# Performance work log

Measured on AMD Instinct MI355X. Metric: run time of the kernel, lower is better.

Reference implementation:

```python
import jax, jax.numpy as jnp
import numpy as np

N = 1_000_000   # total points across all frames in batch
B = 8           # frames (segments) per batch
C = 256         # bottleneck / backbone_out_channels
H = 512         # lstm_hidden_channels
NUM_CLASSES = 20


def setup_inputs() -> dict:
    key = jax.random.key(0)
    ks = jax.random.split(key, 10)
    s = lambda k, shape, scale=0.02: jax.random.normal(k, shape, dtype=jnp.float32) * scale
    feat = jax.random.normal(ks[0], (N, C), dtype=jnp.float32)
    # cumulative offsets: equal-size segments ending at N (torch offset convention)
    offset = (jnp.arange(1, B + 1, dtype=jnp.int32) * (N // B)).astype(jnp.int32)
    return {
        "feat": feat,
        "offset": offset,
        "W_ih": s(ks[1], (4 * H, C)),
        "b_ih": s(ks[2], (4 * H,)),
        "W_hh": s(ks[3], (4 * H, H)),
        "b_hh": s(ks[4], (4 * H,)),
        "W_proj": s(ks[5], (C, H)),
        "b_proj": s(ks[6], (C,)),
        "W_head": s(ks[7], (NUM_CLASSES, C)),
        "b_head": s(ks[8], (NUM_CLASSES,)),
    }


def reference(feat, offset, W_ih, b_ih, W_hh, b_hh, W_proj, b_proj, W_head, b_head):
    n = feat.shape[0]
    # --- ragged per-segment mean pooling (replaces Python loop over offsets) ---
    seg_id = jnp.searchsorted(offset, jnp.arange(n, dtype=offset.dtype), side="right")
    counts = offset - jnp.concatenate([jnp.zeros((1,), offset.dtype), offset[:-1]])
    sums = jax.ops.segment_sum(feat, seg_id, num_segments=offset.shape[0])  # [B, C]
    pooled = sums / counts[:, None].astype(feat.dtype)                      # [B, C]
    # --- LSTMCell with zero initial (h, c): torch gate order i, f, g, o ---
    gates = pooled @ W_ih.T + b_ih + b_hh                                   # h0 = 0 -> W_hh term drops
    i, f, g, o = jnp.split(gates, 4, axis=-1)
    c = jax.nn.sigmoid(i) * jnp.tanh(g)                                     # f * c0 = 0
    h = jax.nn.sigmoid(o) * jnp.tanh(c)                                     # [B, H]
    _ = jax.nn.sigmoid(f)  # f gate unused with zero cell state (kept implicit)
    # --- temporal projection + broadcast fuse (dropout p=0 in eval) ---
    ctx = h @ W_proj.T + b_proj                                             # [B, C]
    fused = feat + ctx[seg_id]                                              # [N, C]
    # --- segmentation head ---
    seg_logits = fused @ W_head.T + b_head                                  # [N, num_classes]
    return seg_logits
```

## Files before the change

### kernel.cpp

```cpp
#include <hip/hip_runtime.h>
#include <math.h>

#define CDIM 256
#define HDIM 512
#define KCLS 20
#define MAXSEG 8
#define TILE_R 64
#define NTHR 512
#define F4_TILE (TILE_R * CDIM / 4)
#define F4_THR (F4_TILE / NTHR)
#define GRIDA 512

__global__ __launch_bounds__(NTHR, 4) void fused_pool_head_kernel(
    const float* __restrict__ feat, const int* __restrict__ offset,
    const float* __restrict__ W_head, const float* __restrict__ b_head,
    float* __restrict__ sums, float* __restrict__ out, int n, int nseg) {
  __shared__ float tile[TILE_R * CDIM];
  float4* tile4 = (float4*)tile;
  int t = threadIdx.x;
  int lane = t & 63;
  int wv = t >> 6;

  int kb_ = (wv < 4) ? wv * 3 : 12 + (wv - 4) * 2;
  int kb = __builtin_amdgcn_readfirstlane(kb_);
  float bh0 = b_head[kb], bh1 = b_head[kb + 1];
  float bh2 = (wv < 4) ? b_head[kb + 2] : 0.f;

  int ntiles = (n + TILE_R - 1) / TILE_R;
  int nb = (int)gridDim.x;
  int t0 = (int)blockIdx.x;

  int off[MAXSEG];
#pragma unroll
  for (int q = 0; q < MAXSEG; ++q) off[q] = (q < nseg) ? offset[q] : 0x7fffffff;

  int col = t & 255;
  int rhalf = (t >> 8) * 32;
  int c4s = col >> 2, js = col & 3;
  float colacc = 0.f;
  int cur_seg = -1;

  const float4* src = (const float4*)feat;
  long lim = (long)n * (CDIM / 4);
  float4 stgA[F4_THR], stgB[F4_THR];

  auto issue = [&](float4* stg, int tl) {
    long base = (long)tl * F4_TILE;
    if (base + F4_TILE <= lim) {
#pragma unroll
      for (int i = 0; i < F4_THR; ++i) stg[i] = src[base + i * NTHR + t];
    } else {
#pragma unroll
      for (int i = 0; i < F4_THR; ++i) {
        long idx = base + i * NTHR + t;
        stg[i] = (idx < lim) ? src[idx] : make_float4(0.f, 0.f, 0.f, 0.f);
      }
    }
  };
  auto dswrite = [&](const float4* stg) {
#pragma unroll
    for (int i = 0; i < F4_THR; ++i) {
      int idx = i * NTHR + t;
      int rr = idx >> 6, c4 = idx & 63;
      tile4[rr * 64 + (c4 ^ (rr & 7))] = stg[i];
    }
  };
  auto compute = [&](int tl) {
    long r0 = (long)tl * TILE_R;
    int rows = (int)(((long)n - r0) < TILE_R ? ((long)n - r0) : TILE_R);

    int rlo = rhalf, rhi = rhalf + 32;
    if (rhi > rows) rhi = rows;
    if (rlo < rhi) {
      long ra = r0 + rlo, rb = r0 + rhi - 1;
      int s0 = 0, s1 = 0;
#pragma unroll
      for (int q = 0; q < MAXSEG - 1; ++q) {
        s0 += (ra >= off[q]) ? 1 : 0;
        s1 += (rb >= off[q]) ? 1 : 0;
      }
      if (s0 == s1) {
        if (s0 != cur_seg) {
          if (cur_seg >= 0) atomicAdd(&sums[cur_seg * CDIM + col], colacc);
          colacc = 0.f;
          cur_seg = s0;
        }
        float a = 0.f;
#pragma unroll 8
        for (int rr = rlo; rr < rhi; ++rr)
          a += tile[(rr * 64 + (c4s ^ (rr & 7))) * 4 + js];
        colacc += a;
      } else {
        for (int rr = rlo; rr < rhi; ++rr) {
          long r = r0 + rr;
          int s = 0;
#pragma unroll
          for (int q = 0; q < MAXSEG - 1; ++q) s += (r >= off[q]) ? 1 : 0;
          if (s != cur_seg) {
            if (cur_seg >= 0) atomicAdd(&sums[cur_seg * CDIM + col], colacc);
            colacc = 0.f;
            cur_seg = s;
          }
          colacc += tile[(rr * 64 + (c4s ^ (rr & 7))) * 4 + js];
        }
      }
    }

    if (lane < rows) {
      const float4* trow = tile4 + lane * 64;
      int l7 = lane & 7;
      if (wv < 4) {
        float a0 = bh0, a1 = bh1, a2 = bh2;
        const float* w0 = W_head + (kb + 0) * CDIM;
        const float* w1 = W_head + (kb + 1) * CDIM;
        const float* w2 = W_head + (kb + 2) * CDIM;
#pragma unroll 4
        for (int c4 = 0; c4 < 64; ++c4) {
          float4 f = trow[c4 ^ l7];
          int cb = c4 * 4;
          a0 = fmaf(f.x, w0[cb], a0); a1 = fmaf(f.x, w1[cb], a1); a2 = fmaf(f.x, w2[cb], a2);
          a0 = fmaf(f.y, w0[cb+1], a0); a1 = fmaf(f.y, w1[cb+1], a1); a2 = fmaf(f.y, w2[cb+1], a2);
          a0 = fmaf(f.z, w0[cb+2], a0); a1 = fmaf(f.z, w1[cb+2], a1); a2 = fmaf(f.z, w2[cb+2], a2);
          a0 = fmaf(f.w, w0[cb+3], a0); a1 = fmaf(f.w, w1[cb+3], a1); a2 = fmaf(f.w, w2[cb+3], a2);
        }
        float* orow = out + (r0 + lane) * KCLS + kb;
        orow[0] = a0; orow[1] = a1; orow[2] = a2;
      } else {
        float a0 = bh0, a1 = bh1;
        const float* w0 = W_head + (kb + 0) * CDIM;
        const float* w1 = W_head + (kb + 1) * CDIM;
#pragma unroll 4
        for (int c4 = 0; c4 < 64; ++c4) {
          float4 f = trow[c4 ^ l7];
          int cb = c4 * 4;
          a0 = fmaf(f.x, w0[cb], a0);   a1 = fmaf(f.x, w1[cb], a1);
          a0 = fmaf(f.y, w0[cb+1], a0); a1 = fmaf(f.y, w1[cb+1], a1);
          a0 = fmaf(f.z, w0[cb+2], a0); a1 = fmaf(f.z, w1[cb+2], a1);
          a0 = fmaf(f.w, w0[cb+3], a0); a1 = fmaf(f.w, w1[cb+3], a1);
        }
        float* orow = out + (r0 + lane) * KCLS + kb;
        orow[0] = a0; orow[1] = a1;
      }
    }
  };

  if (t0 < ntiles) issue(stgA, t0);
  if (t0 + nb < ntiles) issue(stgB, t0 + nb);
  if (t0 < ntiles) dswrite(stgA);
  __syncthreads();

  for (int tl = t0; tl < ntiles; tl += 2 * nb) {
    int tA2 = tl + 2 * nb;
    if (tA2 < ntiles) issue(stgA, tA2);
    compute(tl);
    __syncthreads();
    int tB = tl + nb;
    if (tB < ntiles) dswrite(stgB);
    __syncthreads();
    if (tB < ntiles) {
      int tB2 = tl + 3 * nb;
      if (tB2 < ntiles) issue(stgB, tB2);
      compute(tB);
      __syncthreads();
      if (tA2 < ntiles) dswrite(stgA);
      __syncthreads();
    }
  }
  if (cur_seg >= 0) atomicAdd(&sums[cur_seg * CDIM + col], colacc);
}

__global__ __launch_bounds__(256) void lstm_h_kernel(
    const float* __restrict__ sums, const int* __restrict__ offset,
    const float* __restrict__ W_ih, const float* __restrict__ b_ih,
    const float* __restrict__ b_hh, float* __restrict__ h, int nseg) {
  __shared__ float pooled[MAXSEG * CDIM];
  int t = threadIdx.x;
  {
    int prev = 0;
    for (int s = 0; s < MAXSEG; ++s) {
      int cur = (s < nseg) ? offset[s] : prev;
      float cnt = (float)(cur - prev);
      float inv = (cnt > 0.f) ? 1.f / cnt : 0.f;
      pooled[s * CDIM + t] = sums[s * CDIM + t] * inv;
      prev = cur;
    }
  }
  __syncthreads();

  int wv = t >> 6, l = t & 63;
  int j = (int)blockIdx.x * 4 + wv;
  int s = l >> 3, ch = l & 7;

  const float4* Wi4 = (const float4*)(W_ih + (size_t)(0 * HDIM + j) * CDIM);
  const float4* Wg4 = (const float4*)(W_ih + (size_t)(2 * HDIM + j) * CDIM);
  const float4* Wo4 = (const float4*)(W_ih + (size_t)(3 * HDIM + j) * CDIM);
  const float4* p4 = (const float4*)(pooled + s * CDIM);

  float di = 0.f, dg = 0.f, dd = 0.f;
#pragma unroll
  for (int i = 0; i < 8; ++i) {
    int c4 = ch * 8 + i;
    float4 p = p4[c4];
    float4 wi = Wi4[c4], wg = Wg4[c4], wo = Wo4[c4];
    di = fmaf(p.x, wi.x, di); di = fmaf(p.y, wi.y, di);
    di = fmaf(p.z, wi.z, di); di = fmaf(p.w, wi.w, di);
    dg = fmaf(p.x, wg.x, dg); dg = fmaf(p.y, wg.y, dg);
    dg = fmaf(p.z, wg.z, dg); dg = fmaf(p.w, wg.w, dg);
    dd = fmaf(p.x, wo.x, dd); dd = fmaf(p.y, wo.y, dd);
    dd = fmaf(p.z, wo.z, dd); dd = fmaf(p.w, wo.w, dd);
  }
#pragma unroll
  for (int m = 1; m < 8; m <<= 1) {
    di += __shfl_xor(di, m);
    dg += __shfl_xor(dg, m);
    dd += __shfl_xor(dd, m);
  }
  if (ch == 0 && s < nseg) {
    di += b_ih[j] + b_hh[j];
    dg += b_ih[2 * HDIM + j] + b_hh[2 * HDIM + j];
    dd += b_ih[3 * HDIM + j] + b_hh[3 * HDIM + j];
    float ig = 1.f / (1.f + expf(-di));
    float gg = tanhf(dg);
    float og = 1.f / (1.f + expf(-dd));
    h[(size_t)s * HDIM + j] = og * tanhf(ig * gg);
  }
}

__global__ __launch_bounds__(256) void ctx_kernel(
    const float* __restrict__ h, const float* __restrict__ W_proj,
    const float* __restrict__ b_proj, float* __restrict__ ctx, int nseg) {
  __shared__ float hs[MAXSEG * HDIM];
  int t = threadIdx.x;
  {
    const float4* hsrc = (const float4*)h;
    float4* hdst = (float4*)hs;
#pragma unroll
    for (int i = 0; i < 4; ++i) hdst[i * 256 + t] = hsrc[i * 256 + t];
  }
  __syncthreads();

  int wv = t >> 6, l = t & 63;
  int col = (int)blockIdx.x * 4 + wv;
  int s = l >> 3, ch = l & 7;

  const float4* Wp4 = (const float4*)(W_proj + (size_t)col * HDIM);
  const float4* h4 = (const float4*)(hs + s * HDIM);
  float acc = 0.f;
#pragma unroll
  for (int i = 0; i < 16; ++i) {
    int j4 = ch * 16 + i;
    float4 hv = h4[j4];
    float4 w = Wp4[j4];
    acc = fmaf(hv.x, w.x, acc); acc = fmaf(hv.y, w.y, acc);
    acc = fmaf(hv.z, w.z, acc); acc = fmaf(hv.w, w.w, acc);
  }
#pragma unroll
  for (int m = 1; m < 8; m <<= 1) acc += __shfl_xor(acc, m);
  if (ch == 0 && s < nseg) ctx[s * CDIM + col] = acc + b_proj[col];
}

__global__ __launch_bounds__(256) void delta_kernel(
    const float* __restrict__ ctx, const float* __restrict__ W_head,
    float* __restrict__ delta, int nseg) {
  __shared__ float cs[MAXSEG * CDIM];
  int t = threadIdx.x;
  {
    const float4* csrc = (const float4*)ctx;
    float4* cdst = (float4*)cs;
#pragma unroll
    for (int i = 0; i < 2; ++i) cdst[i * 256 + t] = csrc[i * 256 + t];
  }
  __syncthreads();

  int wv = t >> 6, l = t & 63;
  int k = (int)blockIdx.x * 4 + wv;
  if (k >= KCLS) return;
  int s = l >> 3, ch = l & 7;

  const float4* Wh4 = (const float4*)(W_head + (size_t)k * CDIM);
  const float4* c4 = (const float4*)(cs + s * CDIM);
  float acc = 0.f;
#pragma unroll
  for (int i = 0; i < 8; ++i) {
    int idx = ch * 8 + i;
    float4 cv = c4[idx];
    float4 w = Wh4[idx];
    acc = fmaf(cv.x, w.x, acc); acc = fmaf(cv.y, w.y, acc);
    acc = fmaf(cv.z, w.z, acc); acc = fmaf(cv.w, w.w, acc);
  }
#pragma unroll
  for (int m = 1; m < 8; m <<= 1) acc += __shfl_xor(acc, m);
  if (ch == 0 && s < nseg) delta[s * KCLS + k] = acc;
}

__global__ __launch_bounds__(256) void add_delta_kernel(
    float* __restrict__ out, const int* __restrict__ offset,
    const float* __restrict__ delta, int n, int nseg) {
  __shared__ float dl[MAXSEG * KCLS];
  int t = threadIdx.x;
  if (t < MAXSEG * KCLS) dl[t] = (t < nseg * KCLS) ? delta[t] : 0.f;
  __syncthreads();

  int off[MAXSEG];
#pragma unroll
  for (int q = 0; q < MAXSEG; ++q) off[q] = (q < nseg) ? offset[q] : 0x7fffffff;

  long tot = (long)n * (KCLS / 4);
  long stride = (long)gridDim.x * 256;
  for (long e4 = (long)blockIdx.x * 256 + t; e4 < tot; e4 += stride) {
    long row = e4 / 5;
    int k0 = (int)(e4 - row * 5) * 4;
    int s = 0;
#pragma unroll
    for (int q = 0; q < MAXSEG - 1; ++q) s += (row >= off[q]) ? 1 : 0;
    float4 v = ((float4*)out)[e4];
    const float* d = &dl[s * KCLS + k0];
    v.x += d[0]; v.y += d[1]; v.z += d[2]; v.w += d[3];
    ((float4*)out)[e4] = v;
  }
}

extern "C" void kernel_launch(void* const* d_in, const int* in_sizes, int n_in,
                              void* d_out, int out_size, void* d_ws, size_t ws_size,
                              hipStream_t stream) {
  const float* feat   = (const float*)d_in[0];
  const int*   offset = (const int*)d_in[1];
  const float* W_ih   = (const float*)d_in[2];
  const float* b_ih   = (const float*)d_in[3];
  const float* b_hh   = (const float*)d_in[5];
  const float* W_proj = (const float*)d_in[6];
  const float* b_proj = (const float*)d_in[7];
  const float* W_head = (const float*)d_in[8];
  const float* b_head = (const float*)d_in[9];
  float* out = (float*)d_out;

  int n = in_sizes[0] / CDIM;
  int nseg = in_sizes[1];
  if (nseg > MAXSEG) nseg = MAXSEG;

  float* ws    = (float*)d_ws;
  float* sums  = ws;
  float* h     = ws + MAXSEG * CDIM;
  float* ctx   = ws + MAXSEG * CDIM + MAXSEG * HDIM;
  float* delta = ctx + MAXSEG * CDIM;

  hipMemsetAsync(sums, 0, MAXSEG * CDIM * sizeof(float), stream);
  fused_pool_head_kernel<<<GRIDA, NTHR, 0, stream>>>(feat, offset, W_head, b_head,
                                                     sums, out, n, nseg);
  lstm_h_kernel<<<128, 256, 0, stream>>>(sums, offset, W_ih, b_ih, b_hh, h, nseg);
  ctx_kernel<<<64, 256, 0, stream>>>(h, W_proj, b_proj, ctx, nseg);
  delta_kernel<<<5, 256, 0, stream>>>(ctx, W_head, delta, nseg);
  add_delta_kernel<<<2048, 256, 0, stream>>>(out, offset, delta, n, nseg);
}
```

Baseline: 367.5 us.

## Double-buffer LDS tiles with one barrier per tile and move pooling to four waves

Replaces the single LDS tile plus two register staging sets with two LDS buffers and one register stage. Each iteration now needs one barrier instead of two, and raw s_barrier/waitcnt calls are used. Column pooling moves off all eight waves onto waves 4-7 only, with float4 accumulation and a full-lane XOR swizzle. The fused kernel's grid drops to 256 blocks with the occupancy hint removed, and the add-delta grid grows to 2560 blocks. The doubled LDS footprint may limit how many blocks fit per CU, and the pooling work now sits unevenly across waves.

After: 681.1 us. 85.3% more time.

```diff
diff --git a/kernel.cpp b/kernel.cpp
--- a/kernel.cpp
+++ b/kernel.cpp
@@ -7,44 +7,54 @@
 #define MAXSEG 8
 #define TILE_R 64
 #define NTHR 512
+#define GRIDA 256
 #define F4_TILE (TILE_R * CDIM / 4)
 #define F4_THR (F4_TILE / NTHR)
-#define GRIDA 512
-
-__global__ __launch_bounds__(NTHR, 4) void fused_pool_head_kernel(
+
+__global__ __launch_bounds__(NTHR) void fused_pool_head_kernel(
     const float* __restrict__ feat, const int* __restrict__ offset,
     const float* __restrict__ W_head, const float* __restrict__ b_head,
     float* __restrict__ sums, float* __restrict__ out, int n, int nseg) {
-  __shared__ float tile[TILE_R * CDIM];
-  float4* tile4 = (float4*)tile;
+  __shared__ float4 tile4[2][F4_TILE];
   int t = threadIdx.x;
   int lane = t & 63;
   int wv = t >> 6;
+
+  int ntiles = (n + TILE_R - 1) / TILE_R;
+  int nb = (int)gridDim.x;
+  int t0 = (int)blockIdx.x;
+  if (t0 >= ntiles) return;
+
+  int off[MAXSEG];
+#pragma unroll
+  for (int q = 0; q < MAXSEG; ++q) off[q] = (q < nseg) ? offset[q] : 0x7fffffff;
 
   int kb_ = (wv < 4) ? wv * 3 : 12 + (wv - 4) * 2;
   int kb = __builtin_amdgcn_readfirstlane(kb_);
   float bh0 = b_head[kb], bh1 = b_head[kb + 1];
   float bh2 = (wv < 4) ? b_head[kb + 2] : 0.f;
 
-  int ntiles = (n + TILE_R - 1) / TILE_R;
-  int nb = (int)gridDim.x;
-  int t0 = (int)blockIdx.x;
-
-  int off[MAXSEG];
-#pragma unroll
-  for (int q = 0; q < MAXSEG; ++q) off[q] = (q < nseg) ? offset[q] : 0x7fffffff;
-
-  int col = t & 255;
-  int rhalf = (t >> 8) * 32;
-  int c4s = col >> 2, js = col & 3;
-  float colacc = 0.f;
+  int c4s = lane;
+  int rg = wv - 4;
+  float4 colacc = make_float4(0.f, 0.f, 0.f, 0.f);
   int cur_seg = -1;
 
   const float4* src = (const float4*)feat;
   long lim = (long)n * (CDIM / 4);
-  float4 stgA[F4_THR], stgB[F4_THR];
-
-  auto issue = [&](float4* stg, int tl) {
+  float4 stg[F4_THR];
+
+  auto flush = [&]() {
+    if (cur_seg >= 0) {
+      float* dst = &sums[cur_seg * CDIM + c4s * 4];
+      atomicAdd(dst + 0, colacc.x);
+      atomicAdd(dst + 1, colacc.y);
+      atomicAdd(dst + 2, colacc.z);
+      atomicAdd(dst + 3, colacc.w);
+      colacc = make_float4(0.f, 0.f, 0.f, 0.f);
+    }
+  };
+
+  auto issue = [&](int tl) {
     long base = (long)tl * F4_TILE;
     if (base + F4_TILE <= lim) {
 #pragma unroll
@@ -57,68 +67,66 @@
       }
     }
   };
-  auto dswrite = [&](const float4* stg) {
+  auto dswrite = [&](int b) {
 #pragma unroll
     for (int i = 0; i < F4_THR; ++i) {
       int idx = i * NTHR + t;
       int rr = idx >> 6, c4 = idx & 63;
-      tile4[rr * 64 + (c4 ^ (rr & 7))] = stg[i];
+      tile4[b][rr * 64 + (c4 ^ rr)] = stg[i];
     }
   };
-  auto compute = [&](int tl) {
+
+  auto compute = [&](int b, int tl) {
     long r0 = (long)tl * TILE_R;
     int rows = (int)(((long)n - r0) < TILE_R ? ((long)n - r0) : TILE_R);
-
-    int rlo = rhalf, rhi = rhalf + 32;
-    if (rhi > rows) rhi = rows;
-    if (rlo < rhi) {
-      long ra = r0 + rlo, rb = r0 + rhi - 1;
-      int s0 = 0, s1 = 0;
-#pragma unroll
-      for (int q = 0; q < MAXSEG - 1; ++q) {
-        s0 += (ra >= off[q]) ? 1 : 0;
-        s1 += (rb >= off[q]) ? 1 : 0;
-      }
-      if (s0 == s1) {
-        if (s0 != cur_seg) {
-          if (cur_seg >= 0) atomicAdd(&sums[cur_seg * CDIM + col], colacc);
-          colacc = 0.f;
-          cur_seg = s0;
+    const float4* t4 = &tile4[b][0];
+
+    if (wv >= 4) {
+      int rlo = rg * 16, rhi = rlo + 16;
+      if (rhi > rows) rhi = rows;
+      if (rlo < rhi) {
+        long ra = r0 + rlo, rb = r0 + rhi - 1;
+        int s0 = 0, s1 = 0;
+#pragma unroll
+        for (int q = 0; q < MAXSEG - 1; ++q) {
+          s0 += (ra >= off[q]) ? 1 : 0;
+          s1 += (rb >= off[q]) ? 1 : 0;
         }
-        float a = 0.f;
-#pragma unroll 8
-        for (int rr = rlo; rr < rhi; ++rr)
-          a += tile[(rr * 64 + (c4s ^ (rr & 7))) * 4 + js];
-        colacc += a;
-      } else {
-        for (int rr = rlo; rr < rhi; ++rr) {
-          long r = r0 + rr;
-          int s = 0;
-#pragma unroll
-          for (int q = 0; q < MAXSEG - 1; ++q) s += (r >= off[q]) ? 1 : 0;
-          if (s != cur_seg) {
-            if (cur_seg >= 0) atomicAdd(&sums[cur_seg * CDIM + col], colacc);
-            colacc = 0.f;
-            cur_seg = s;
+        if (s0 == s1) {
+          if (s0 != cur_seg) { flush(); cur_seg = s0; }
+          float4 a = make_float4(0.f, 0.f, 0.f, 0.f);
+#pragma unroll
+          for (int rr = rlo; rr < rhi; ++rr) {
+            float4 v = t4[rr * 64 + (c4s ^ rr)];
+            a.x += v.x; a.y += v.y; a.z += v.z; a.w += v.w;
           }
-          colacc += tile[(rr * 64 + (c4s ^ (rr & 7))) * 4 + js];
+          colacc.x += a.x; colacc.y += a.y; colacc.z += a.z; colacc.w += a.w;
+        } else {
+          for (int rr = rlo; rr < rhi; ++rr) {
+            long r = r0 + rr;
+            int s = 0;
+#pragma unroll
+            for (int q = 0; q < MAXSEG - 1; ++q) s += (r >= off[q]) ? 1 : 0;
+            if (s != cur_seg) { flush(); cur_seg = s; }
+            float4 v = t4[rr * 64 + (c4s ^ rr)];
+            colacc.x += v.x; colacc.y += v.y; colacc.z += v.z; colacc.w += v.w;
+          }
         }
       }
     }
 
     if (lane < rows) {
-      const float4* trow = tile4 + lane * 64;
-      int l7 = lane & 7;
+      const float4* trow = t4 + lane * 64;
       if (wv < 4) {
         float a0 = bh0, a1 = bh1, a2 = bh2;
-        const float* w0 = W_head + (kb + 0) * CDIM;
-        const float* w1 = W_head + (kb + 1) * CDIM;
-        const float* w2 = W_head + (kb + 2) * CDIM;
+        const float* w0 = W_head + (size_t)(kb + 0) * CDIM;
+        const float* w1 = W_head + (size_t)(kb + 1) * CDIM;
+        const float* w2 = W_head + (size_t)(kb + 2) * CDIM;
 #pragma unroll 4
         for (int c4 = 0; c4 < 64; ++c4) {
-          float4 f = trow[c4 ^ l7];
+          float4 f = trow[c4 ^ lane];
           int cb = c4 * 4;
-          a0 = fmaf(f.x, w0[cb], a0); a1 = fmaf(f.x, w1[cb], a1); a2 = fmaf(f.x, w2[cb], a2);
+          a0 = fmaf(f.x, w0[cb], a0);   a1 = fmaf(f.x, w1[cb], a1);   a2 = fmaf(f.x, w2[cb], a2);
           a0 = fmaf(f.y, w0[cb+1], a0); a1 = fmaf(f.y, w1[cb+1], a1); a2 = fmaf(f.y, w2[cb+1], a2);
           a0 = fmaf(f.z, w0[cb+2], a0); a1 = fmaf(f.z, w1[cb+2], a1); a2 = fmaf(f.z, w2[cb+2], a2);
           a0 = fmaf(f.w, w0[cb+3], a0); a1 = fmaf(f.w, w1[cb+3], a1); a2 = fmaf(f.w, w2[cb+3], a2);
@@ -127,11 +135,11 @@
         orow[0] = a0; orow[1] = a1; orow[2] = a2;
       } else {
         float a0 = bh0, a1 = bh1;
-        const float* w0 = W_head + (kb + 0) * CDIM;
-        const float* w1 = W_head + (kb + 1) * CDIM;
+        const float* w0 = W_head + (size_t)(kb + 0) * CDIM;
+        const float* w1 = W_head + (size_t)(kb + 1) * CDIM;
 #pragma unroll 4
         for (int c4 = 0; c4 < 64; ++c4) {
-          float4 f = trow[c4 ^ l7];
+          float4 f = trow[c4 ^ lane];
           int cb = c4 * 4;
           a0 = fmaf(f.x, w0[cb], a0);   a1 = fmaf(f.x, w1[cb], a1);
           a0 = fmaf(f.y, w0[cb+1], a0); a1 = fmaf(f.y, w1[cb+1], a1);
@@ -144,29 +152,28 @@
     }
   };
 
-  if (t0 < ntiles) issue(stgA, t0);
-  if (t0 + nb < ntiles) issue(stgB, t0 + nb);
-  if (t0 < ntiles) dswrite(stgA);
-  __syncthreads();
-
-  for (int tl = t0; tl < ntiles; tl += 2 * nb) {
-    int tA2 = tl + 2 * nb;
-    if (tA2 < ntiles) issue(stgA, tA2);
-    compute(tl);
-    __syncthreads();
-    int tB = tl + nb;
-    if (tB < ntiles) dswrite(stgB);
-    __syncthreads();
-    if (tB < ntiles) {
-      int tB2 = tl + 3 * nb;
-      if (tB2 < ntiles) issue(stgB, tB2);
-      compute(tB);
-      __syncthreads();
-      if (tA2 < ntiles) dswrite(stgA);
-      __syncthreads();
-    }
-  }
-  if (cur_seg >= 0) atomicAdd(&sums[cur_seg * CDIM + col], colacc);
+  issue(t0);
+  dswrite(0);
+  if (t0 + nb < ntiles) issue(t0 + nb);
+  asm volatile("s_waitcnt lgkmcnt(0)" ::: "memory");
+  __builtin_amdgcn_s_barrier();
+  __builtin_amdgcn_sched_barrier(0);
+
+  int cur = 0;
+  for (int tl = t0; tl < ntiles; tl += nb) {
+    compute(cur, tl);
+    int t1 = tl + nb;
+    if (t1 < ntiles) {
+      dswrite(cur ^ 1);
+      int t2 = t1 + nb;
+      if (t2 < ntiles) issue(t2);
+    }
+    asm volatile("s_waitcnt lgkmcnt(0)" ::: "memory");
+    __builtin_amdgcn_s_barrier();
+    __builtin_amdgcn_sched_barrier(0);
+    cur ^= 1;
+  }
+  flush();
 }
 
 __global__ __launch_bounds__(256) void lstm_h_kernel(
@@ -350,5 +357,5 @@
   lstm_h_kernel<<<128, 256, 0, stream>>>(sums, offset, W_ih, b_ih, b_hh, h, nseg);
   ctx_kernel<<<64, 256, 0, stream>>>(h, W_proj, b_proj, ctx, nseg);
   delta_kernel<<<5, 256, 0, stream>>>(ctx, W_head, delta, nseg);
-  add_delta_kernel<<<2048, 256, 0, stream>>>(out, offset, delta, n, nseg);
-}
+  add_delta_kernel<<<2560, 256, 0, stream>>>(out, offset, delta, n, nseg);
+}
```
